# Kernel tuning notes

Hardware: AMD Instinct MI355X
Metric: run time of the kernel (lower is better)

Reference implementation:

```python
import jax, jax.numpy as jnp
import numpy as np

N = 50000      # nodes
E = 800000     # edges
F = 128        # node feature dim (= output_size, residual)
H = 128        # hidden_size

def _uniform_fan_avg(key, shape):
    # VarianceScaling(scale=1.0, mode='fan_avg', distribution='uniform')
    fan_avg = (shape[0] + shape[1]) / 2.0
    limit = np.sqrt(3.0 / fan_avg)
    return jax.random.uniform(key, shape, jnp.float32, -limit, limit)

def setup_inputs() -> dict:
    key = jax.random.key(0)
    ks = jax.random.split(key, 16)
    h = jax.random.normal(ks[0], (N, F), jnp.float32)
    pos = jax.random.normal(ks[1], (N, 3), jnp.float32)
    senders = jax.random.randint(ks[2], (E,), 0, N, jnp.int32)
    receivers = jax.random.randint(ks[3], (E,), 0, N, jnp.int32)
    # edge_mlp: Linear(2F+1 -> H) silu, Linear(H -> H) silu (activate_final=True)
    eW1 = _uniform_fan_avg(ks[4], (2 * F + 1, H)); eb1 = jnp.zeros((H,), jnp.float32)
    eW2 = _uniform_fan_avg(ks[5], (H, H)); eb2 = jnp.zeros((H,), jnp.float32)
    # node_mlp: Linear(F+H -> H) silu, Linear(H -> F) (no final act)
    nW1 = _uniform_fan_avg(ks[6], (F + H, H)); nb1 = jnp.zeros((H,), jnp.float32)
    nW2 = _uniform_fan_avg(ks[7], (H, F)); nb2 = jnp.zeros((F,), jnp.float32)
    # pos_correction_mlp: Linear(H -> H) silu, Linear(H -> 1, no bias, UniformScaling(dt))
    pW1 = _uniform_fan_avg(ks[8], (H, H)); pb1 = jnp.zeros((H,), jnp.float32)
    dt = 0.001
    pW2 = jax.random.uniform(ks[9], (H, 1), jnp.float32, -dt, dt) * np.sqrt(3.0)
    return {"h": h, "pos": pos, "senders": senders, "receivers": receivers,
            "eW1": eW1, "eb1": eb1, "eW2": eW2, "eb2": eb2,
            "nW1": nW1, "nb1": nb1, "nW2": nW2, "nb2": nb2,
            "pW1": pW1, "pb1": pb1, "pW2": pW2}

def reference(h, pos, senders, receivers,
              eW1, eb1, eW2, eb2,
              nW1, nb1, nW2, nb2,
              pW1, pb1, pW2):
    n = h.shape[0]
    # _coord2radial (normalize=False)
    coord_diff = pos[senders] - pos[receivers]            # [E,3]
    radial = jnp.sum(coord_diff ** 2, axis=1, keepdims=True)  # [E,1]
    # edge update (_message): concat(h[senders], h[receivers], radial) -> edge_mlp
    msg_in = jnp.concatenate([h[senders], h[receivers], radial], axis=-1)  # [E,2F+1]
    msg = jax.nn.silu(msg_in @ eW1 + eb1)
    msg = jax.nn.silu(msg @ eW2 + eb2)                    # [E,H]
    # node update (_update): aggregate messages at receivers, node_mlp, residual
    agg = jax.ops.segment_sum(msg, receivers, num_segments=n)  # [N,H]
    x = jnp.concatenate([h, agg], axis=-1)                # [N,F+H]
    x = jax.nn.silu(x @ nW1 + nb1)
    x = x @ nW2 + nb2                                     # [N,F]
    h_new = h + x                                         # residual
    # position update (_pos_update)
    pc = jax.nn.silu(msg @ pW1 + pb1) @ pW2               # [E,1]
    trans = jnp.clip(coord_diff * pc, -100, 100)          # [E,3]
    pos_new = pos + jax.ops.segment_sum(trans, senders, num_segments=n)
    return h_new, pos_new
```

## Files before the change

### kernel.cpp

```cpp
#include <hip/hip_runtime.h>
#include <hip/hip_bf16.h>

#define NNODES 50000
#define NEDGES 800000
#define EB 1024
#define SCAN_BLOCKS 196

typedef short bf16x8 __attribute__((ext_vector_type(8)));
typedef float f32x4 __attribute__((ext_vector_type(4)));
typedef unsigned short u16;
typedef unsigned int u32;

union U4 { ushort4 v; u16 a[4]; };

__device__ __forceinline__ u16 f2bf(float f) {
    __hip_bfloat16 b = __float2bfloat16(f);
    return *reinterpret_cast<u16*>(&b);
}
__device__ __forceinline__ float bf2f(u16 v) {
    u32 u = ((u32)v) << 16;
    return __uint_as_float(u);
}
__device__ __forceinline__ float silu(float x) {
    return x / (1.0f + __expf(-x));
}
__device__ __forceinline__ bf16x8 ld8(const u16* p) {
    return *(const bf16x8*)p;
}
__device__ __forceinline__ f32x4 mfma16(bf16x8 a, bf16x8 b, f32x4 c) {
    return __builtin_amdgcn_mfma_f32_16x16x32_bf16(a, b, c, 0, 0, 0);
}

__global__ void transpose_cvt(const float* __restrict__ src, u16* __restrict__ dst,
                              int K, int N) {
    int i = blockIdx.x * 256 + threadIdx.x;
    if (i < K * N) {
        int n = i / K;
        int k = i - n * K;
        dst[i] = f2bf(src[k * N + n]);
    }
}

__global__ __launch_bounds__(256) void gemm_p(
    const float* __restrict__ h, const u16* __restrict__ eW1T,
    const u16* __restrict__ nW1T, u16* __restrict__ P)
{
    const int tid  = threadIdx.x;
    const int w    = tid >> 6;
    const int lane = tid & 63;
    const int m    = lane & 15;
    const int quad = lane >> 4;
    const int ksub = quad * 8;

    bf16x8 bw[4][6];
    #pragma unroll
    for (int cc = 0; cc < 6; cc++) {
        int C = 96 * w + 16 * cc + m;
        const u16* bp;
        if (C < 128)      bp = eW1T + C * 256;
        else if (C < 256) bp = eW1T + (C - 128) * 256 + 128;
        else              bp = nW1T + (C - 256) * 256;
        #pragma unroll
        for (int t = 0; t < 4; t++) bw[t][cc] = ld8(bp + t * 32 + ksub);
    }
    const int base = blockIdx.x * 64;
    #pragma unroll
    for (int mt = 0; mt < 4; mt++) {
        int nm = base + mt * 16 + m;
        if (nm >= NNODES) nm = NNODES - 1;
        bf16x8 afr[4];
        #pragma unroll
        for (int t = 0; t < 4; t++) {
            const float* ap = h + (size_t)nm * 128 + t * 32 + ksub;
            f32x4 lo = *(const f32x4*)ap;
            f32x4 hi = *(const f32x4*)(ap + 4);
            #pragma unroll
            for (int j = 0; j < 4; j++) {
                afr[t][j]     = (short)f2bf(lo[j]);
                afr[t][4 + j] = (short)f2bf(hi[j]);
            }
        }
        f32x4 acc[6];
        #pragma unroll
        for (int cc = 0; cc < 6; cc++) acc[cc] = (f32x4){0,0,0,0};
        #pragma unroll
        for (int t = 0; t < 4; t++)
            #pragma unroll
            for (int cc = 0; cc < 6; cc++)
                acc[cc] = mfma16(afr[t], bw[t][cc], acc[cc]);
        #pragma unroll
        for (int cc = 0; cc < 6; cc++) {
            int C = 96 * w + 16 * cc + m;
            #pragma unroll
            for (int r = 0; r < 4; r++) {
                int nr = base + mt * 16 + quad * 4 + r;
                if (nr < NNODES) P[(size_t)nr * 384 + C] = f2bf(acc[cc][r]);
            }
        }
    }
}

__global__ void hist_kernel(const int* __restrict__ rcv, int* __restrict__ counts) {
    int e = blockIdx.x * 256 + threadIdx.x;
    if (e < NEDGES) atomicAdd(&counts[rcv[e]], 1);
}
__global__ void scan1(const int* __restrict__ counts, int* __restrict__ excl,
                      int* __restrict__ blkSum) {
    __shared__ int tmp[256];
    int tx = threadIdx.x;
    int i = blockIdx.x * 256 + tx;
    int v = (i < NNODES) ? counts[i] : 0;
    tmp[tx] = v;
    __syncthreads();
    for (int off = 1; off < 256; off <<= 1) {
        int t = (tx >= off) ? tmp[tx - off] : 0;
        __syncthreads();
        tmp[tx] += t;
        __syncthreads();
    }
    if (i < NNODES) excl[i] = tmp[tx] - v;
    if (tx == 255) blkSum[blockIdx.x] = tmp[255];
}
__global__ void scan2(const int* __restrict__ blkSum, int* __restrict__ blkOff) {
    __shared__ int tmp[256];
    int tx = threadIdx.x;
    int v = (tx < SCAN_BLOCKS) ? blkSum[tx] : 0;
    tmp[tx] = v;
    __syncthreads();
    for (int off = 1; off < 256; off <<= 1) {
        int t = (tx >= off) ? tmp[tx - off] : 0;
        __syncthreads();
        tmp[tx] += t;
        __syncthreads();
    }
    if (tx < SCAN_BLOCKS) blkOff[tx] = tmp[tx] - v;
}
__global__ void scan3(const int* __restrict__ excl, const int* __restrict__ blkOff,
                      int* __restrict__ cursor) {
    int i = blockIdx.x * 256 + threadIdx.x;
    if (i < NNODES) cursor[i] = excl[i] + blkOff[blockIdx.x];
}
__global__ void scatter_kernel(const int* __restrict__ rcv, int* __restrict__ cursor,
                               int* __restrict__ perm) {
    int e = blockIdx.x * 256 + threadIdx.x;
    if (e < NEDGES) {
        int p = atomicAdd(&cursor[rcv[e]], 1);
        perm[p] = e;
    }
}

struct __align__(16) EdgeLds {
    u16   m1[64 * 136];
    u16   msg[64 * 136];
    int   snd[64];
    int   rcvloc[64];
    float radial[64];
    float diff[64][4];
    float pcpart[4][64];
    float wlast[128];
    float b1[128];
};

__global__ __launch_bounds__(256, 4) void edge_kernel(
    const u16* __restrict__ P, const float* __restrict__ pos,
    const int* __restrict__ snd, const int* __restrict__ rcv,
    const int* __restrict__ perm,
    const float* __restrict__ eW1last, const float* __restrict__ eb1,
    const u16* __restrict__ eW2T, const float* __restrict__ eb2,
    const u16* __restrict__ pW1T, const float* __restrict__ pb1,
    const float* __restrict__ pW2,
    float* __restrict__ agg, float* __restrict__ posacc)
{
    __shared__ EdgeLds S;
    const int tid  = threadIdx.x;
    const int w    = tid >> 6;
    const int lane = tid & 63;
    const int m    = lane & 15;
    const int quad = lane >> 4;
    const int ksub = quad * 8;

    bf16x8 bw2[4][2], bp1[4][2];
    float b2v[2], pb1v[2], pw2v[2];
    #pragma unroll
    for (int cc = 0; cc < 2; cc++) {
        int col = (2 * w + cc) * 16 + m;
        #pragma unroll
        for (int t = 0; t < 4; t++) {
            bw2[t][cc] = ld8(eW2T + col * 128 + t * 32 + ksub);
            bp1[t][cc] = ld8(pW1T + col * 128 + t * 32 + ksub);
        }
        b2v[cc]  = eb2[col];
        pb1v[cc] = pb1[col];
        pw2v[cc] = pW2[col];
    }
    if (tid < 128) { S.wlast[tid] = eW1last[tid]; S.b1[tid] = eb1[tid]; }

    for (int base = blockIdx.x * 64; base < NEDGES; base += gridDim.x * 64) {
        __syncthreads();
        if (tid < 64) {
            int e = perm[base + tid];
            int s = snd[e], r = rcv[e];
            S.snd[tid] = s; S.rcvloc[tid] = r;
            float rad = 0.f;
            #pragma unroll
            for (int c = 0; c < 3; c++) {
                float d = pos[s * 3 + c] - pos[r * 3 + c];
                S.diff[tid][c] = d;
                rad += d * d;
            }
            S.radial[tid] = rad;
        }
        __syncthreads();
        #pragma unroll
        for (int k = 0; k < 8; k++) {
            int cid = tid + k * 256;
            int e = cid >> 5;
            int p = cid & 31;
            int s = S.snd[e], r = S.rcvloc[e];
            float rad = S.radial[e];
            U4 pa, pb, o;
            pa.v = *(const ushort4*)(P + (size_t)s * 384 + p * 4);
            pb.v = *(const ushort4*)(P + (size_t)r * 384 + 128 + p * 4);
            #pragma unroll
            for (int j = 0; j < 4; j++) {
                int col = p * 4 + j;
                float v = bf2f(pa.a[j]) + bf2f(pb.a[j]) + rad * S.wlast[col] + S.b1[col];
                o.a[j] = f2bf(silu(v));
            }
            *(ushort4*)&S.m1[e * 136 + p * 4] = o.v;
        }
        __syncthreads();
        #pragma unroll
        for (int mt = 0; mt < 4; mt++) {
            f32x4 acc0 = (f32x4){0,0,0,0}, acc1 = (f32x4){0,0,0,0};
            #pragma unroll
            for (int t = 0; t < 4; t++) {
                bf16x8 a = *(const bf16x8*)&S.m1[(mt * 16 + m) * 136 + t * 32 + ksub];
                acc0 = mfma16(a, bw2[t][0], acc0);
                acc1 = mfma16(a, bw2[t][1], acc1);
            }
            #pragma unroll
            for (int cc = 0; cc < 2; cc++) {
                f32x4 acc = cc ? acc1 : acc0;
                int col = (2 * w + cc) * 16 + m;
                #pragma unroll
                for (int r = 0; r < 4; r++) {
                    int row = mt * 16 + quad * 4 + r;
                    S.msg[row * 136 + col] = f2bf(silu(acc[r] + b2v[cc]));
                }
            }
        }
        __syncthreads();
        #pragma unroll
        for (int mt = 0; mt < 4; mt++) {
            f32x4 acc0 = (f32x4){0,0,0,0}, acc1 = (f32x4){0,0,0,0};
            #pragma unroll
            for (int t = 0; t < 4; t++) {
                bf16x8 a = *(const bf16x8*)&S.msg[(mt * 16 + m) * 136 + t * 32 + ksub];
                acc0 = mfma16(a, bp1[t][0], acc0);
                acc1 = mfma16(a, bp1[t][1], acc1);
            }
            float p4[4];
            #pragma unroll
            for (int r = 0; r < 4; r++)
                p4[r] = silu(acc0[r] + pb1v[0]) * pw2v[0]
                      + silu(acc1[r] + pb1v[1]) * pw2v[1];
            #pragma unroll
            for (int mask = 1; mask < 16; mask <<= 1) {
                #pragma unroll
                for (int r = 0; r < 4; r++) p4[r] += __shfl_xor(p4[r], mask);
            }
            if (m == 0) {
                #pragma unroll
                for (int r = 0; r < 4; r++)
                    S.pcpart[w][mt * 16 + quad * 4 + r] = p4[r];
            }
        }
        {
            int half = tid >> 7, col = tid & 127;
            int r0 = half * 32;
            float a = 0.f;
            int cur = S.rcvloc[r0];
            for (int r = r0; r < r0 + 32; ++r) {
                int rc = S.rcvloc[r];
                if (rc != cur) {
                    atomicAdd(&agg[(size_t)cur * 128 + col], a);
                    a = 0.f; cur = rc;
                }
                a += bf2f(S.msg[r * 136 + col]);
            }
            atomicAdd(&agg[(size_t)cur * 128 + col], a);
        }
        __syncthreads();
        if (tid < 192) {
            int e = tid / 3, c = tid - e * 3;
            float pc = S.pcpart[0][e] + S.pcpart[1][e] + S.pcpart[2][e] + S.pcpart[3][e];
            float tr = S.diff[e][c] * pc;
            tr = fminf(fmaxf(tr, -100.f), 100.f);
            atomicAdd(&posacc[S.snd[e] * 3 + c], tr);
        }
    }
}

__global__ __launch_bounds__(256, 4) void node_kernel(
    const u16* __restrict__ P, const float* __restrict__ h,
    const float* __restrict__ agg,
    const u16* __restrict__ nW1T, const float* __restrict__ nb1,
    const u16* __restrict__ nW2T, const float* __restrict__ nb2,
    float* __restrict__ out)
{
    __shared__ alignas(16) u16 m1[64 * 136];
    const int tid  = threadIdx.x;
    const int w    = tid >> 6;
    const int lane = tid & 63;
    const int m    = lane & 15;
    const int quad = lane >> 4;
    const int ksub = quad * 8;

    bf16x8 bw1[4][2], bw2[4][2];
    float b1v[2], b2v[2];
    #pragma unroll
    for (int cc = 0; cc < 2; cc++) {
        int col = (2 * w + cc) * 16 + m;
        #pragma unroll
        for (int t = 0; t < 4; t++) {
            bw1[t][cc] = ld8(nW1T + col * 256 + 128 + t * 32 + ksub);
            bw2[t][cc] = ld8(nW2T + col * 128 + t * 32 + ksub);
        }
        b1v[cc] = nb1[col];
        b2v[cc] = nb2[col];
    }
    const int base = blockIdx.x * 64;
    #pragma unroll
    for (int mt = 0; mt < 4; mt++) {
        int nm = base + mt * 16 + m;
        if (nm >= NNODES) nm = NNODES - 1;
        f32x4 acc0 = (f32x4){0,0,0,0}, acc1 = (f32x4){0,0,0,0};
        #pragma unroll
        for (int t = 0; t < 4; t++) {
            const float* ap = agg + (size_t)nm * 128 + t * 32 + ksub;
            f32x4 lo = *(const f32x4*)ap;
            f32x4 hi = *(const f32x4*)(ap + 4);
            bf16x8 a;
            #pragma unroll
            for (int j = 0; j < 4; j++) {
                a[j]     = (short)f2bf(lo[j]);
                a[4 + j] = (short)f2bf(hi[j]);
            }
            acc0 = mfma16(a, bw1[t][0], acc0);
            acc1 = mfma16(a, bw1[t][1], acc1);
        }
        #pragma unroll
        for (int cc = 0; cc < 2; cc++) {
            f32x4 acc = cc ? acc1 : acc0;
            int col = (2 * w + cc) * 16 + m;
            #pragma unroll
            for (int r = 0; r < 4; r++) {
                int row = mt * 16 + quad * 4 + r;
                int nrc = base + row; if (nrc >= NNODES) nrc = NNODES - 1;
                float v = acc[r] + bf2f(P[(size_t)nrc * 384 + 256 + col]) + b1v[cc];
                m1[row * 136 + col] = f2bf(silu(v));
            }
        }
    }
    __syncthreads();
    #pragma unroll
    for (int mt = 0; mt < 4; mt++) {
        f32x4 acc0 = (f32x4){0,0,0,0}, acc1 = (f32x4){0,0,0,0};
        #pragma unroll
        for (int t = 0; t < 4; t++) {
            bf16x8 a = *(const bf16x8*)&m1[(mt * 16 + m) * 136 + t * 32 + ksub];
            acc0 = mfma16(a, bw2[t][0], acc0);
            acc1 = mfma16(a, bw2[t][1], acc1);
        }
        #pragma unroll
        for (int cc = 0; cc < 2; cc++) {
            f32x4 acc = cc ? acc1 : acc0;
            int col = (2 * w + cc) * 16 + m;
            #pragma unroll
            for (int r = 0; r < 4; r++) {
                int nr = base + mt * 16 + quad * 4 + r;
                if (nr < NNODES)
                    out[(size_t)nr * 128 + col] = acc[r] + b2v[cc] + h[(size_t)nr * 128 + col];
            }
        }
    }
}

__global__ void pos_kernel(const float* __restrict__ pos,
                           const float* __restrict__ posacc,
                           float* __restrict__ out) {
    int i = blockIdx.x * 256 + threadIdx.x;
    if (i < NNODES * 3) {
        out[NNODES * 128 + i] = pos[i] + posacc[i];
    }
}

extern "C" void kernel_launch(void* const* d_in, const int* in_sizes, int n_in,
                              void* d_out, int out_size, void* d_ws, size_t ws_size,
                              hipStream_t stream) {
    (void)in_sizes; (void)n_in; (void)out_size; (void)ws_size;
    const float* h   = (const float*)d_in[0];
    const float* pos = (const float*)d_in[1];
    const int*   snd = (const int*)d_in[2];
    const int*   rcv = (const int*)d_in[3];
    const float* eW1 = (const float*)d_in[4];
    const float* eb1 = (const float*)d_in[5];
    const float* eW2 = (const float*)d_in[6];
    const float* eb2 = (const float*)d_in[7];
    const float* nW1 = (const float*)d_in[8];
    const float* nb1 = (const float*)d_in[9];
    const float* nW2 = (const float*)d_in[10];
    const float* nb2 = (const float*)d_in[11];
    const float* pW1 = (const float*)d_in[12];
    const float* pb1 = (const float*)d_in[13];
    const float* pW2 = (const float*)d_in[14];
    float* out = (float*)d_out;

    float* agg    = (float*)d_ws;
    float* posacc = agg + (size_t)NNODES * 128;
    u16* P    = (u16*)(posacc + (size_t)NNODES * 3);
    u16* eW1T = P + (size_t)NNODES * 384;
    u16* eW2T = eW1T + 128 * 256;
    u16* pW1T = eW2T + 128 * 128;
    u16* nW1T = pW1T + 128 * 128;
    u16* nW2T = nW1T + 128 * 256;
    int* counts = (int*)(nW2T + 128 * 128);
    int* excl   = counts + 50048;
    int* blkSum = excl + 50048;
    int* blkOff = blkSum + 256;
    int* cursor = blkOff + 256;
    int* perm   = cursor + 50048;

    hipMemsetAsync(agg, 0, (size_t)NNODES * 131 * sizeof(float), stream);
    hipMemsetAsync(counts, 0, 50048 * sizeof(int), stream);

    transpose_cvt<<<(256 * 128 + 255) / 256, 256, 0, stream>>>(eW1, eW1T, 256, 128);
    transpose_cvt<<<(128 * 128 + 255) / 256, 256, 0, stream>>>(eW2, eW2T, 128, 128);
    transpose_cvt<<<(128 * 128 + 255) / 256, 256, 0, stream>>>(pW1, pW1T, 128, 128);
    transpose_cvt<<<(256 * 128 + 255) / 256, 256, 0, stream>>>(nW1, nW1T, 256, 128);
    transpose_cvt<<<(128 * 128 + 255) / 256, 256, 0, stream>>>(nW2, nW2T, 128, 128);

    gemm_p<<<(NNODES + 63) / 64, 256, 0, stream>>>(h, eW1T, nW1T, P);

    hist_kernel<<<(NEDGES + 255) / 256, 256, 0, stream>>>(rcv, counts);
    scan1<<<SCAN_BLOCKS, 256, 0, stream>>>(counts, excl, blkSum);
    scan2<<<1, 256, 0, stream>>>(blkSum, blkOff);
    scan3<<<SCAN_BLOCKS, 256, 0, stream>>>(excl, blkOff, cursor);
    scatter_kernel<<<(NEDGES + 255) / 256, 256, 0, stream>>>(rcv, cursor, perm);

    edge_kernel<<<EB, 256, 0, stream>>>(
        P, pos, snd, rcv, perm,
        eW1 + 256 * 128, eb1,
        eW2T, eb2, pW1T, pb1, pW2,
        agg, posacc);

    node_kernel<<<(NNODES + 63) / 64, 256, 0, stream>>>(
        P, h, agg, nW1T, nb1, nW2T, nb2, out);

    pos_kernel<<<(NNODES * 3 + 255) / 256, 256, 0, stream>>>(pos, posacc, out);
}
```

Before: 516.0 us.

## Fuse prep kernels, fold edge bias into gemm, vectorize and swizzle edge gather

The five weight transposes and the receiver histogram are merged into one prep kernel, and the position output kernel is folded into the node kernel, which cuts launch count. The first edge-layer bias is split in half and folded into the per-node precomputed projections. The edge gather is restructured so each wave loads 16-byte chunks per edge and writes them into shared memory with an XOR swizzle, meant to avoid bank conflicts on the MFMA A-operand reads. SiLU switches to exp2/rcp intrinsics, which lowers arithmetic cost at some cost in precision.

```diff
diff --git a/kernel.cpp b/kernel.cpp
--- a/kernel.cpp
+++ b/kernel.cpp
@@ -5,14 +5,13 @@
 #define NEDGES 800000
 #define EB 1024
 #define SCAN_BLOCKS 196
+#define TRN_BLOCKS 448
 
 typedef short bf16x8 __attribute__((ext_vector_type(8)));
 typedef float f32x4 __attribute__((ext_vector_type(4)));
 typedef unsigned short u16;
 typedef unsigned int u32;
 
-union U4 { ushort4 v; u16 a[4]; };
-
 __device__ __forceinline__ u16 f2bf(float f) {
     __hip_bfloat16 b = __float2bfloat16(f);
     return *reinterpret_cast<u16*>(&b);
@@ -21,8 +20,13 @@
     u32 u = ((u32)v) << 16;
     return __uint_as_float(u);
 }
-__device__ __forceinline__ float silu(float x) {
-    return x / (1.0f + __expf(-x));
+__device__ __forceinline__ u32 pack2(float a, float b) {
+    __hip_bfloat162 t = __float22bfloat162_rn(float2{a, b});
+    return *reinterpret_cast<u32*>(&t);
+}
+__device__ __forceinline__ float fast_silu(float x) {
+    float e = __builtin_amdgcn_exp2f(-1.442695040888963f * x);
+    return x * __builtin_amdgcn_rcpf(1.0f + e);
 }
 __device__ __forceinline__ bf16x8 ld8(const u16* p) {
     return *(const bf16x8*)p;
@@ -31,19 +35,34 @@
     return __builtin_amdgcn_mfma_f32_16x16x32_bf16(a, b, c, 0, 0, 0);
 }
 
-__global__ void transpose_cvt(const float* __restrict__ src, u16* __restrict__ dst,
-                              int K, int N) {
-    int i = blockIdx.x * 256 + threadIdx.x;
-    if (i < K * N) {
-        int n = i / K;
-        int k = i - n * K;
-        dst[i] = f2bf(src[k * N + n]);
+__global__ void prep_kernel(const float* __restrict__ eW1, const float* __restrict__ eW2,
+                            const float* __restrict__ pW1, const float* __restrict__ nW1,
+                            const float* __restrict__ nW2,
+                            u16* __restrict__ eW1T, u16* __restrict__ eW2T,
+                            u16* __restrict__ pW1T, u16* __restrict__ nW1T,
+                            u16* __restrict__ nW2T,
+                            const int* __restrict__ rcv, int* __restrict__ counts) {
+    int b = blockIdx.x;
+    if (b < TRN_BLOCKS) {
+        int i = b * 256 + threadIdx.x;
+        const float* src; u16* dst; int K;
+        if (i < 32768)      { src = eW1; dst = eW1T; K = 256; }
+        else if (i < 49152) { src = eW2; dst = eW2T; K = 128; i -= 32768; }
+        else if (i < 65536) { src = pW1; dst = pW1T; K = 128; i -= 49152; }
+        else if (i < 98304) { src = nW1; dst = nW1T; K = 256; i -= 65536; }
+        else                { src = nW2; dst = nW2T; K = 128; i -= 98304; }
+        int n = i / K, k = i - n * K;
+        dst[i] = f2bf(src[k * 128 + n]);
+    } else {
+        int e = (b - TRN_BLOCKS) * 256 + threadIdx.x;
+        if (e < NEDGES) atomicAdd(&counts[rcv[e]], 1);
     }
 }
 
 __global__ __launch_bounds__(256) void gemm_p(
     const float* __restrict__ h, const u16* __restrict__ eW1T,
-    const u16* __restrict__ nW1T, u16* __restrict__ P)
+    const u16* __restrict__ nW1T, const float* __restrict__ eb1,
+    u16* __restrict__ P)
 {
     const int tid  = threadIdx.x;
     const int w    = tid >> 6;
@@ -53,13 +72,14 @@
     const int ksub = quad * 8;
 
     bf16x8 bw[4][6];
+    float bias[6];
     #pragma unroll
     for (int cc = 0; cc < 6; cc++) {
         int C = 96 * w + 16 * cc + m;
         const u16* bp;
-        if (C < 128)      bp = eW1T + C * 256;
-        else if (C < 256) bp = eW1T + (C - 128) * 256 + 128;
-        else              bp = nW1T + (C - 256) * 256;
+        if (C < 128)      { bp = eW1T + C * 256;               bias[cc] = 0.5f * eb1[C]; }
+        else if (C < 256) { bp = eW1T + (C - 128) * 256 + 128; bias[cc] = 0.5f * eb1[C - 128]; }
+        else              { bp = nW1T + (C - 256) * 256;       bias[cc] = 0.f; }
         #pragma unroll
         for (int t = 0; t < 4; t++) bw[t][cc] = ld8(bp + t * 32 + ksub);
     }
@@ -94,16 +114,12 @@
             #pragma unroll
             for (int r = 0; r < 4; r++) {
                 int nr = base + mt * 16 + quad * 4 + r;
-                if (nr < NNODES) P[(size_t)nr * 384 + C] = f2bf(acc[cc][r]);
-            }
-        }
-    }
-}
-
-__global__ void hist_kernel(const int* __restrict__ rcv, int* __restrict__ counts) {
-    int e = blockIdx.x * 256 + threadIdx.x;
-    if (e < NEDGES) atomicAdd(&counts[rcv[e]], 1);
-}
+                if (nr < NNODES) P[(size_t)nr * 384 + C] = f2bf(acc[cc][r] + bias[cc]);
+            }
+        }
+    }
+}
+
 __global__ void scan1(const int* __restrict__ counts, int* __restrict__ excl,
                       int* __restrict__ blkSum) {
     __shared__ int tmp[256];
@@ -152,20 +168,19 @@
 struct __align__(16) EdgeLds {
     u16   m1[64 * 136];
     u16   msg[64 * 136];
-    int   snd[64];
-    int   rcvloc[64];
-    float radial[64];
     float diff[64][4];
     float pcpart[4][64];
     float wlast[128];
-    float b1[128];
+    float radial[64];
+    int   sndloc[64];
+    int   rcvloc[64];
 };
 
 __global__ __launch_bounds__(256, 4) void edge_kernel(
     const u16* __restrict__ P, const float* __restrict__ pos,
     const int* __restrict__ snd, const int* __restrict__ rcv,
     const int* __restrict__ perm,
-    const float* __restrict__ eW1last, const float* __restrict__ eb1,
+    const float* __restrict__ eW1last,
     const u16* __restrict__ eW2T, const float* __restrict__ eb2,
     const u16* __restrict__ pW1T, const float* __restrict__ pb1,
     const float* __restrict__ pW2,
@@ -193,14 +208,15 @@
         pb1v[cc] = pb1[col];
         pw2v[cc] = pW2[col];
     }
-    if (tid < 128) { S.wlast[tid] = eW1last[tid]; S.b1[tid] = eb1[tid]; }
+    if (tid < 128) S.wlast[tid] = eW1last[tid];
 
     for (int base = blockIdx.x * 64; base < NEDGES; base += gridDim.x * 64) {
         __syncthreads();
+        const int e = lane;
+        int eg = perm[base + e];
+        int s = snd[eg], r = rcv[eg];
         if (tid < 64) {
-            int e = perm[base + tid];
-            int s = snd[e], r = rcv[e];
-            S.snd[tid] = s; S.rcvloc[tid] = r;
+            S.sndloc[tid] = s; S.rcvloc[tid] = r;
             float rad = 0.f;
             #pragma unroll
             for (int c = 0; c < 3; c++) {
@@ -211,31 +227,38 @@
             S.radial[tid] = rad;
         }
         __syncthreads();
-        #pragma unroll
-        for (int k = 0; k < 8; k++) {
-            int cid = tid + k * 256;
-            int e = cid >> 5;
-            int p = cid & 31;
-            int s = S.snd[e], r = S.rcvloc[e];
+        {
             float rad = S.radial[e];
-            U4 pa, pb, o;
-            pa.v = *(const ushort4*)(P + (size_t)s * 384 + p * 4);
-            pb.v = *(const ushort4*)(P + (size_t)r * 384 + 128 + p * 4);
-            #pragma unroll
-            for (int j = 0; j < 4; j++) {
-                int col = p * 4 + j;
-                float v = bf2f(pa.a[j]) + bf2f(pb.a[j]) + rad * S.wlast[col] + S.b1[col];
-                o.a[j] = f2bf(silu(v));
-            }
-            *(ushort4*)&S.m1[e * 136 + p * 4] = o.v;
+            const u16* pa = P + (size_t)s * 384 + w * 32;
+            const u16* pb = P + (size_t)r * 384 + 128 + w * 32;
+            const int sw = e >> 3;
+            #pragma unroll
+            for (int k = 0; k < 4; k++) {
+                bf16x8 va = ld8(pa + k * 8);
+                bf16x8 vb = ld8(pb + k * 8);
+                u32 pk[4];
+                #pragma unroll
+                for (int jj = 0; jj < 4; jj++) {
+                    int col = w * 32 + k * 8 + jj * 2;
+                    float2 wl = *(const float2*)&S.wlast[col];
+                    float v0 = bf2f((u16)va[jj * 2])     + bf2f((u16)vb[jj * 2])     + rad * wl.x;
+                    float v1 = bf2f((u16)va[jj * 2 + 1]) + bf2f((u16)vb[jj * 2 + 1]) + rad * wl.y;
+                    pk[jj] = pack2(fast_silu(v0), fast_silu(v1));
+                }
+                int chunk = (w * 4 + k) ^ sw;
+                *(uint4*)&S.m1[e * 136 + chunk * 8] =
+                    make_uint4(pk[0], pk[1], pk[2], pk[3]);
+            }
         }
         __syncthreads();
         #pragma unroll
         for (int mt = 0; mt < 4; mt++) {
+            const int rs = mt * 2 + (m >> 3);
+            const int row = mt * 16 + m;
             f32x4 acc0 = (f32x4){0,0,0,0}, acc1 = (f32x4){0,0,0,0};
             #pragma unroll
             for (int t = 0; t < 4; t++) {
-                bf16x8 a = *(const bf16x8*)&S.m1[(mt * 16 + m) * 136 + t * 32 + ksub];
+                bf16x8 a = *(const bf16x8*)&S.m1[row * 136 + ((t * 4 + quad) ^ rs) * 8];
                 acc0 = mfma16(a, bw2[t][0], acc0);
                 acc1 = mfma16(a, bw2[t][1], acc1);
             }
@@ -244,9 +267,9 @@
                 f32x4 acc = cc ? acc1 : acc0;
                 int col = (2 * w + cc) * 16 + m;
                 #pragma unroll
-                for (int r = 0; r < 4; r++) {
-                    int row = mt * 16 + quad * 4 + r;
-                    S.msg[row * 136 + col] = f2bf(silu(acc[r] + b2v[cc]));
+                for (int rr = 0; rr < 4; rr++) {
+                    int orow = mt * 16 + quad * 4 + rr;
+                    S.msg[orow * 136 + col] = f2bf(fast_silu(acc[rr] + b2v[cc]));
                 }
             }
         }
@@ -262,18 +285,18 @@
             }
             float p4[4];
             #pragma unroll
-            for (int r = 0; r < 4; r++)
-                p4[r] = silu(acc0[r] + pb1v[0]) * pw2v[0]
-                      + silu(acc1[r] + pb1v[1]) * pw2v[1];
+            for (int rr = 0; rr < 4; rr++)
+                p4[rr] = fast_silu(acc0[rr] + pb1v[0]) * pw2v[0]
+                       + fast_silu(acc1[rr] + pb1v[1]) * pw2v[1];
             #pragma unroll
             for (int mask = 1; mask < 16; mask <<= 1) {
                 #pragma unroll
-                for (int r = 0; r < 4; r++) p4[r] += __shfl_xor(p4[r], mask);
+                for (int rr = 0; rr < 4; rr++) p4[rr] += __shfl_xor(p4[rr], mask);
             }
             if (m == 0) {
                 #pragma unroll
-                for (int r = 0; r < 4; r++)
-                    S.pcpart[w][mt * 16 + quad * 4 + r] = p4[r];
+                for (int rr = 0; rr < 4; rr++)
+                    S.pcpart[w][mt * 16 + quad * 4 + rr] = p4[rr];
             }
         }
         {
@@ -281,23 +304,23 @@
             int r0 = half * 32;
             float a = 0.f;
             int cur = S.rcvloc[r0];
-            for (int r = r0; r < r0 + 32; ++r) {
-                int rc = S.rcvloc[r];
+            for (int rr = r0; rr < r0 + 32; ++rr) {
+                int rc = S.rcvloc[rr];
                 if (rc != cur) {
                     atomicAdd(&agg[(size_t)cur * 128 + col], a);
                     a = 0.f; cur = rc;
                 }
-                a += bf2f(S.msg[r * 136 + col]);
+                a += bf2f(S.msg[rr * 136 + col]);
             }
             atomicAdd(&agg[(size_t)cur * 128 + col], a);
         }
         __syncthreads();
         if (tid < 192) {
-            int e = tid / 3, c = tid - e * 3;
-            float pc = S.pcpart[0][e] + S.pcpart[1][e] + S.pcpart[2][e] + S.pcpart[3][e];
-            float tr = S.diff[e][c] * pc;
+            int ee = tid / 3, c = tid - ee * 3;
+            float pc = S.pcpart[0][ee] + S.pcpart[1][ee] + S.pcpart[2][ee] + S.pcpart[3][ee];
+            float tr = S.diff[ee][c] * pc;
             tr = fminf(fmaxf(tr, -100.f), 100.f);
-            atomicAdd(&posacc[S.snd[e] * 3 + c], tr);
+            atomicAdd(&posacc[S.sndloc[ee] * 3 + c], tr);
         }
     }
 }
@@ -307,6 +330,7 @@
     const float* __restrict__ agg,
     const u16* __restrict__ nW1T, const float* __restrict__ nb1,
     const u16* __restrict__ nW2T, const float* __restrict__ nb2,
+    const float* __restrict__ pos, const float* __restrict__ posacc,
     float* __restrict__ out)
 {
     __shared__ alignas(16) u16 m1[64 * 136];
@@ -355,11 +379,11 @@
             f32x4 acc = cc ? acc1 : acc0;
             int col = (2 * w + cc) * 16 + m;
             #pragma unroll
-            for (int r = 0; r < 4; r++) {
-                int row = mt * 16 + quad * 4 + r;
+            for (int rr = 0; rr < 4; rr++) {
+                int row = mt * 16 + quad * 4 + rr;
                 int nrc = base + row; if (nrc >= NNODES) nrc = NNODES - 1;
-                float v = acc[r] + bf2f(P[(size_t)nrc * 384 + 256 + col]) + b1v[cc];
-                m1[row * 136 + col] = f2bf(silu(v));
+                float v = acc[rr] + bf2f(P[(size_t)nrc * 384 + 256 + col]) + b1v[cc];
+                m1[row * 136 + col] = f2bf(fast_silu(v));
             }
         }
     }
@@ -378,21 +402,16 @@
             f32x4 acc = cc ? acc1 : acc0;
             int col = (2 * w + cc) * 16 + m;
             #pragma unroll
-            for (int r = 0; r < 4; r++) {
-                int nr = base + mt * 16 + quad * 4 + r;
+            for (int rr = 0; rr < 4; rr++) {
+                int nr = base + mt * 16 + quad * 4 + rr;
                 if (nr < NNODES)
-                    out[(size_t)nr * 128 + col] = acc[r] + b2v[cc] + h[(size_t)nr * 128 + col];
-            }
-        }
-    }
-}
-
-__global__ void pos_kernel(const float* __restrict__ pos,
-                           const float* __restrict__ posacc,
-                           float* __restrict__ out) {
-    int i = blockIdx.x * 256 + threadIdx.x;
-    if (i < NNODES * 3) {
-        out[NNODES * 128 + i] = pos[i] + posacc[i];
+                    out[(size_t)nr * 128 + col] = acc[rr] + b2v[cc] + h[(size_t)nr * 128 + col];
+            }
+        }
+    }
+    if (tid < 192) {
+        int i = blockIdx.x * 192 + tid;
+        if (i < NNODES * 3) out[NNODES * 128 + i] = pos[i] + posacc[i];
     }
 }
 
@@ -435,15 +454,11 @@
     hipMemsetAsync(agg, 0, (size_t)NNODES * 131 * sizeof(float), stream);
     hipMemsetAsync(counts, 0, 50048 * sizeof(int), stream);
 
-    transpose_cvt<<<(256 * 128 + 255) / 256, 256, 0, stream>>>(eW1, eW1T, 256, 128);
-    transpose_cvt<<<(128 * 128 + 255) / 256, 256, 0, stream>>>(eW2, eW2T, 128, 128);
-    transpose_cvt<<<(128 * 128 + 255) / 256, 256, 0, stream>>>(pW1, pW1T, 128, 128);
-    transpose_cvt<<<(256 * 128 + 255) / 256, 256, 0, stream>>>(nW1, nW1T, 256, 128);
-    transpose_cvt<<<(128 * 128 + 255) / 256, 256, 0, stream>>>(nW2, nW2T, 128, 128);
-
-    gemm_p<<<(NNODES + 63) / 64, 256, 0, stream>>>(h, eW1T, nW1T, P);
-
-    hist_kernel<<<(NEDGES + 255) / 256, 256, 0, stream>>>(rcv, counts);
+    prep_kernel<<<TRN_BLOCKS + (NEDGES + 255) / 256, 256, 0, stream>>>(
+        eW1, eW2, pW1, nW1, nW2, eW1T, eW2T, pW1T, nW1T, nW2T, rcv, counts);
+
+    gemm_p<<<(NNODES + 63) / 64, 256, 0, stream>>>(h, eW1T, nW1T, eb1, P);
+
     scan1<<<SCAN_BLOCKS, 256, 0, stream>>>(counts, excl, blkSum);
     scan2<<<1, 256, 0, stream>>>(blkSum, blkOff);
     scan3<<<SCAN_BLOCKS, 256, 0, stream>>>(excl, blkOff, cursor);
@@ -451,12 +466,10 @@
 
     edge_kernel<<<EB, 256, 0, stream>>>(
         P, pos, snd, rcv, perm,
-        eW1 + 256 * 128, eb1,
+        eW1 + 256 * 128,
         eW2T, eb2, pW1T, pb1, pW2,
         agg, posacc);
 
     node_kernel<<<(NNODES + 63) / 64, 256, 0, stream>>>(
-        P, h, agg, nW1T, nb1, nW2T, nb2, out);
-
-    pos_kernel<<<(NNODES * 3 + 255) / 256, 256, 0, stream>>>(pos, posacc, out);
-}
+        P, h, agg, nW1T, nb1, nW2T, nb2, pos, posacc, out);
+}
```

After: 449.8 us. 12.8% less time.
